# Performance work log

Hardware: AMD Instinct MI355X
Metric: run time of the kernel (lower is better)

Reference implementation:

```python
import jax, jax.numpy as jnp
import numpy as np

LABEL_SMOOTHING = 0.1
K_SLOPE = 5.0
N, D = 8192, 256


def setup_inputs() -> dict:
    key = jax.random.key(0)
    k1, k2, k3 = jax.random.split(key, 3)
    return {
        "image_features1": jax.random.normal(k1, (N, D), dtype=jnp.float32),
        "image_features2": jax.random.normal(k2, (N, D), dtype=jnp.float32),
        "logit_scale": jnp.asarray(14.2857, dtype=jnp.float32),  # ~ 1/0.07 CLIP temp
        "positive_weights": jax.random.normal(k3, (N,), dtype=jnp.float32),
    }


def _l2_normalize(x, axis=-1, eps=1e-12):
    # matches F.normalize(dim=-1)
    norm = jnp.linalg.norm(x, axis=axis, keepdims=True)
    return x / jnp.maximum(norm, eps)


def _weighted_infonce(sim, eps):
    # per row i: (1-eps_i)*(-sim[i,i] + lse_i) + eps_i*(-mean(sim[i,:]) + lse_i)
    #          = lse_i - (1-eps_i)*sim[i,i] - eps_i*mean_i
    n = sim.shape[0]
    lse = jax.nn.logsumexp(sim, axis=1)            # [n]
    diag = jnp.diagonal(sim)                       # [n]
    row_mean = jnp.mean(sim, axis=1)               # [n]
    per_row = lse - (1.0 - eps) * diag - eps * row_mean
    return jnp.sum(per_row) / n


def reference(image_features1, image_features2, logit_scale, positive_weights):
    f1 = _l2_normalize(image_features1)
    f2 = _l2_normalize(image_features2)
    logits12 = logit_scale * (f1 @ f2.T)           # [N, N]
    # eps = 1 - (1 - label_smoothing) * sigmoid(k * w)
    eps = 1.0 - (1.0 - LABEL_SMOOTHING) * jax.nn.sigmoid(K_SLOPE * positive_weights)
    loss1 = _weighted_infonce(logits12, eps)
    loss2 = _weighted_infonce(logits12.T, eps)
    return (loss1 + loss2) / 2.0
```

## Files before the change

kernel.cpp:

```cpp
#include <hip/hip_runtime.h>
#include <hip/hip_bf16.h>

#define NN 8192
#define DD 256
#define LOG2E 1.4426950408889634f
#define LN2f 0.6931471805599453f

typedef __attribute__((ext_vector_type(8))) short short8;
typedef __attribute__((ext_vector_type(4))) float f32x4;

__device__ __forceinline__ unsigned short f2bf(float x) {
    unsigned int u = __float_as_uint(x);
    u += 0x7fff + ((u >> 16) & 1);
    return (unsigned short)(u >> 16);
}
__device__ __forceinline__ float epsf(float w) {
    return 1.f - 0.9f / (1.f + __expf(-5.f * w));
}

__global__ __launch_bounds__(512) void nrm_kernel(
    const float* __restrict__ f1, const float* __restrict__ f2,
    const float* __restrict__ scale_p, const float* __restrict__ wts,
    unsigned short* __restrict__ f1n, unsigned short* __restrict__ f2n,
    float* __restrict__ diag, float* __restrict__ rse, float* __restrict__ cse,
    float4* __restrict__ STp, float* __restrict__ totalp)
{
    __shared__ float4 red[8][256];
    const int w = threadIdx.x >> 6, lane = threadIdx.x & 63;
    const float s = scale_p[0];
    const int row0 = blockIdx.x * 16 + w * 2;
    float s1a[4] = {0,0,0,0}, t1a[4] = {0,0,0,0};
    float s2a[4] = {0,0,0,0}, t2a[4] = {0,0,0,0};
#pragma unroll
    for (int r = 0; r < 2; ++r) {
        const int row = row0 + r;
        const float4 a = reinterpret_cast<const float4*>(f1 + (size_t)row * DD)[lane];
        const float4 b = reinterpret_cast<const float4*>(f2 + (size_t)row * DD)[lane];
        float sa = a.x * a.x + a.y * a.y + a.z * a.z + a.w * a.w;
        float sb = b.x * b.x + b.y * b.y + b.z * b.z + b.w * b.w;
        float sab = a.x * b.x + a.y * b.y + a.z * b.z + a.w * b.w;
#pragma unroll
        for (int off = 1; off < 64; off <<= 1) {
            sa += __shfl_xor(sa, off);
            sb += __shfl_xor(sb, off);
            sab += __shfl_xor(sab, off);
        }
        const float n1 = fmaxf(sqrtf(sa), 1e-12f);
        const float n2 = fmaxf(sqrtf(sb), 1e-12f);
        const float e = epsf(wts[row]);
        if (lane == 0) { diag[row] = s * sab / (n1 * n2); rse[row] = 0.f; cse[row] = 0.f; }
        const float r1 = s * LOG2E / n1, r2 = 1.0f / n2;
        const float v0 = a.x * r1, v1 = a.y * r1, v2 = a.z * r1, v3 = a.w * r1;
        const float u0 = b.x * r2, u1 = b.y * r2, u2 = b.z * r2, u3 = b.w * r2;
        ushort4 o1, o2;
        o1.x = f2bf(v0); o1.y = f2bf(v1); o1.z = f2bf(v2); o1.w = f2bf(v3);
        o2.x = f2bf(u0); o2.y = f2bf(u1); o2.z = f2bf(u2); o2.w = f2bf(u3);
        reinterpret_cast<ushort4*>(f1n + (size_t)row * DD)[lane] = o1;
        reinterpret_cast<ushort4*>(f2n + (size_t)row * DD)[lane] = o2;
        s1a[0] += v0; s1a[1] += v1; s1a[2] += v2; s1a[3] += v3;
        t1a[0] += e * v0; t1a[1] += e * v1; t1a[2] += e * v2; t1a[3] += e * v3;
        s2a[0] += u0; s2a[1] += u1; s2a[2] += u2; s2a[3] += u3;
        t2a[0] += e * u0; t2a[1] += e * u1; t2a[2] += e * u2; t2a[3] += e * u3;
    }
#pragma unroll
    for (int k = 0; k < 4; ++k)
        red[w][lane * 4 + k] = make_float4(s1a[k], t1a[k], s2a[k], t2a[k]);
    __syncthreads();
    if (threadIdx.x < 256) {
        const int c = threadIdx.x;
        float4 acc = red[0][c];
#pragma unroll
        for (int q = 1; q < 8; ++q) {
            const float4 v = red[q][c];
            acc.x += v.x; acc.y += v.y; acc.z += v.z; acc.w += v.w;
        }
        STp[blockIdx.x * 256 + c] = acc;
    }
    if (blockIdx.x == 0 && threadIdx.x == 0) totalp[0] = 0.f;
}

__global__ __launch_bounds__(256, 2) void gemm_kernel(
    const unsigned short* __restrict__ f1n, const unsigned short* __restrict__ f2n,
    float* __restrict__ rowsumexp, float* __restrict__ colsumexp)
{
    __shared__ char Bs[2][64 * 512];
    __shared__ float colbuf[2][1024];
    const int bid = blockIdx.x;
    const int bm = bid >> 3, bc = bid & 7;
    const int w = threadIdx.x >> 6, lane = threadIdx.x & 63;
    const int wr = (w >> 1) * 64, wc = (w & 1) * 32;
    const int lhi = lane >> 4, llo = lane & 15;

    const char* aBase = (const char*)f1n + ((size_t)(bm * 128 + wr + llo) * 512) + lhi * 16;
    short8 av[4][8];
#pragma unroll
    for (int m = 0; m < 4; ++m)
#pragma unroll
        for (int ks = 0; ks < 8; ++ks)
            av[m][ks] = *(const short8*)(aBase + (size_t)(m * 16) * 512 + ks * 64);
#pragma unroll
    for (int m = 0; m < 4; ++m)
#pragma unroll
        for (int ks = 0; ks < 8; ++ks)
            asm volatile("" : "+v"(av[m][ks]));

    const char* bBase = (const char*)f2n + (size_t)bc * 1024 * 512;

    auto stage = [&](int buf, int tile) {
#pragma unroll
        for (int i = 0; i < 8; ++i) {
            const int r = w * 16 + i * 2 + (lane >> 5);
            const int cs = (lane & 31) ^ (r & 15);
            __builtin_amdgcn_global_load_lds(
                (const __attribute__((address_space(1))) unsigned int*)
                    (bBase + (size_t)(tile * 64 + r) * 512 + cs * 16),
                (__attribute__((address_space(3))) unsigned int*)
                    (&Bs[buf][(w * 16 + i * 2) * 512]), 16, 0, 0);
        }
    };

    float rowpart[16];
#pragma unroll
    for (int i = 0; i < 16; ++i) rowpart[i] = 0.f;

    stage(0, 0);

    const int rb0 = wc + llo, rb1 = wc + 16 + llo;
    const int sw = llo << 4;

    for (int t = 0; t < 16; ++t) {
        const int cur = t & 1;
        if (t < 15) {
            stage(cur ^ 1, t + 1);
            asm volatile("s_waitcnt vmcnt(8)" ::: "memory");
        } else {
            asm volatile("s_waitcnt vmcnt(0)" ::: "memory");
        }
        __builtin_amdgcn_s_barrier();
        __builtin_amdgcn_sched_barrier(0);

        f32x4 acc[4][2];
#pragma unroll
        for (int m = 0; m < 4; ++m) {
            acc[m][0] = (f32x4){0.f, 0.f, 0.f, 0.f};
            acc[m][1] = (f32x4){0.f, 0.f, 0.f, 0.f};
        }
        const char* bs = Bs[cur];
#pragma unroll
        for (int ks = 0; ks < 8; ++ks) {
            const int kb = ks * 64 + lhi * 16;
            const short8 bv0 = *(const short8*)(bs + rb0 * 512 + (kb ^ sw));
            const short8 bv1 = *(const short8*)(bs + rb1 * 512 + (kb ^ sw));
#pragma unroll
            for (int m = 0; m < 4; ++m) {
                acc[m][0] = __builtin_amdgcn_mfma_f32_16x16x32_bf16(av[m][ks], bv0, acc[m][0], 0, 0, 0);
                acc[m][1] = __builtin_amdgcn_mfma_f32_16x16x32_bf16(av[m][ks], bv1, acc[m][1], 0, 0, 0);
            }
        }

        float cee0 = 0.f, cee1 = 0.f;
#pragma unroll
        for (int m = 0; m < 4; ++m)
#pragma unroll
            for (int j = 0; j < 4; ++j) {
                const float e0 = __builtin_exp2f(acc[m][0][j]);
                const float e1 = __builtin_exp2f(acc[m][1][j]);
                rowpart[m * 4 + j] += e0 + e1;
                cee0 += e0; cee1 += e1;
            }
        cee0 += __shfl_xor(cee0, 16); cee0 += __shfl_xor(cee0, 32);
        cee1 += __shfl_xor(cee1, 16); cee1 += __shfl_xor(cee1, 32);
        if (lhi == 0) {
            colbuf[w >> 1][t * 64 + wc + llo] = cee0;
            colbuf[w >> 1][t * 64 + wc + 16 + llo] = cee1;
        }
        __builtin_amdgcn_s_barrier();
    }

    __syncthreads();

#pragma unroll
    for (int m = 0; m < 4; ++m)
#pragma unroll
        for (int j = 0; j < 4; ++j) {
            float v = rowpart[m * 4 + j];
            v += __shfl_xor(v, 1); v += __shfl_xor(v, 2);
            v += __shfl_xor(v, 4); v += __shfl_xor(v, 8);
            if (llo == 0)
                atomicAdd(&rowsumexp[bm * 128 + wr + m * 16 + lhi * 4 + j], v);
        }
    for (int c = threadIdx.x; c < 1024; c += 256)
        atomicAdd(&colsumexp[bc * 1024 + c], colbuf[0][c] + colbuf[1][c]);
}

__global__ __launch_bounds__(256) void finA_kernel(
    const float* __restrict__ rse, const float* __restrict__ cse,
    const float* __restrict__ diag, const float* __restrict__ wts,
    const float4* __restrict__ STp, float4* __restrict__ P2,
    float* __restrict__ totalp)
{
    const int g = blockIdx.x, t = threadIdx.x;
    const int i = g * 256 + t;
    const float eps = epsf(wts[i]);
    float a = __logf(rse[i]) + __logf(cse[i]) - 2.f * (1.f - eps) * diag[i];
#pragma unroll
    for (int off = 1; off < 64; off <<= 1) a += __shfl_xor(a, off);
    __shared__ float red[4];
    if ((t & 63) == 0) red[t >> 6] = a;

    float4 s = make_float4(0.f, 0.f, 0.f, 0.f);
#pragma unroll 4
    for (int j = 0; j < 16; ++j) {
        const float4 v = STp[(g * 16 + j) * 256 + t];
        s.x += v.x; s.y += v.y; s.z += v.z; s.w += v.w;
    }
    P2[g * 256 + t] = s;

    __syncthreads();
    if (t == 0) atomicAdd(totalp, red[0] + red[1] + red[2] + red[3]);
}

__global__ __launch_bounds__(256) void fin_kernel(
    const float4* __restrict__ P2, const float* __restrict__ totalp,
    float* __restrict__ out)
{
    const int t = threadIdx.x;
    float4 s = make_float4(0.f, 0.f, 0.f, 0.f);
#pragma unroll 4
    for (int g = 0; g < 32; ++g) {
        const float4 v = P2[g * 256 + t];
        s.x += v.x; s.y += v.y; s.z += v.z; s.w += v.w;
    }
    float d = (s.y * s.z + s.x * s.w) * (LN2f / (float)NN);
#pragma unroll
    for (int off = 1; off < 64; off <<= 1) d += __shfl_xor(d, off);
    __shared__ float red[4];
    if ((t & 63) == 0) red[t >> 6] = d;
    __syncthreads();
    if (t == 0) {
        const float dot = red[0] + red[1] + red[2] + red[3];
        out[0] = (totalp[0] - dot) * (1.f / (2.f * (float)NN));
    }
}

extern "C" void kernel_launch(void* const* d_in, const int* in_sizes, int n_in,
                              void* d_out, int out_size, void* d_ws, size_t ws_size,
                              hipStream_t stream) {
    (void)in_sizes; (void)n_in; (void)out_size; (void)ws_size;
    const float* f1 = (const float*)d_in[0];
    const float* f2 = (const float*)d_in[1];
    const float* scale = (const float*)d_in[2];
    const float* wts = (const float*)d_in[3];
    float* out = (float*)d_out;

    char* ws = (char*)d_ws;
    unsigned short* f1n = (unsigned short*)ws;
    unsigned short* f2n = (unsigned short*)(ws + (size_t)4 * 1024 * 1024);
    float* fb = (float*)(ws + (size_t)8 * 1024 * 1024);
    float* rse    = fb;
    float* cse    = fb + 8192;
    float* diag   = fb + 16384;
    float* totalp = fb + 24576;
    float4* STp   = (float4*)(fb + 32768);
    float4* P2    = (float4*)(fb + 32768 + 524288);

    nrm_kernel<<<512, 512, 0, stream>>>(f1, f2, scale, wts, f1n, f2n,
                                        diag, rse, cse, STp, totalp);
    gemm_kernel<<<512, 256, 0, stream>>>(f1n, f2n, rse, cse);
    finA_kernel<<<32, 256, 0, stream>>>(rse, cse, diag, wts, STp, P2, totalp);
    fin_kernel<<<1, 256, 0, stream>>>(P2, totalp, out);
}
```

Baseline: 69.30 us.

## Give each wave a private B-tile pipeline to drop block-wide barriers

Each of the four waves now stages its own 16-row B sub-tile into a private double-buffered LDS slot and walks its own half of the block's 1024 columns across 32 steps. This removes the two per-iteration s_barrier calls and lets waves run independently, with loads issued two tiles ahead. In exchange the two waves sharing a column half each load B separately, and only one B fragment feeds the MFMA chain per step, so the MFMA-to-LDS-read ratio drops and global/LDS traffic for B doubles.

```diff
diff --git a/kernel.cpp b/kernel.cpp
--- a/kernel.cpp
+++ b/kernel.cpp
@@ -83,15 +83,16 @@
     const unsigned short* __restrict__ f1n, const unsigned short* __restrict__ f2n,
     float* __restrict__ rowsumexp, float* __restrict__ colsumexp)
 {
-    __shared__ char Bs[2][64 * 512];
+    __shared__ char Bs[4][2][16 * 512];
     __shared__ float colbuf[2][1024];
     const int bid = blockIdx.x;
     const int bm = bid >> 3, bc = bid & 7;
     const int w = threadIdx.x >> 6, lane = threadIdx.x & 63;
-    const int wr = (w >> 1) * 64, wc = (w & 1) * 32;
+    const int h = w >> 1;
+    const int cst = w & 1;
     const int lhi = lane >> 4, llo = lane & 15;
 
-    const char* aBase = (const char*)f1n + ((size_t)(bm * 128 + wr + llo) * 512) + lhi * 16;
+    const char* aBase = (const char*)f1n + ((size_t)(bm * 128 + h * 64 + llo) * 512) + lhi * 16;
     short8 av[4][8];
 #pragma unroll
     for (int m = 0; m < 4; ++m)
@@ -104,18 +105,20 @@
         for (int ks = 0; ks < 8; ++ks)
             asm volatile("" : "+v"(av[m][ks]));
 
-    const char* bBase = (const char*)f2n + (size_t)bc * 1024 * 512;
+    const char* bBase = (const char*)f2n + (size_t)(bc * 1024 + cst * 512) * 512;
 
     auto stage = [&](int buf, int tile) {
+        char* dst = &Bs[w][buf][0];
+        const char* src = bBase + (size_t)(tile * 16) * 512;
 #pragma unroll
         for (int i = 0; i < 8; ++i) {
-            const int r = w * 16 + i * 2 + (lane >> 5);
-            const int cs = (lane & 31) ^ (r & 15);
+            const int r = i * 2 + (lane >> 5);
+            const int cs = (lane & 31) ^ r;
             __builtin_amdgcn_global_load_lds(
                 (const __attribute__((address_space(1))) unsigned int*)
-                    (bBase + (size_t)(tile * 64 + r) * 512 + cs * 16),
+                    (src + (size_t)r * 512 + cs * 16),
                 (__attribute__((address_space(3))) unsigned int*)
-                    (&Bs[buf][(w * 16 + i * 2) * 512]), 16, 0, 0);
+                    (dst + i * 2 * 512), 16, 0, 0);
         }
     };
 
@@ -124,57 +127,43 @@
     for (int i = 0; i < 16; ++i) rowpart[i] = 0.f;
 
     stage(0, 0);
-
-    const int rb0 = wc + llo, rb1 = wc + 16 + llo;
+    stage(1, 1);
+
     const int sw = llo << 4;
 
-    for (int t = 0; t < 16; ++t) {
-        const int cur = t & 1;
-        if (t < 15) {
-            stage(cur ^ 1, t + 1);
+    for (int t = 0; t < 32; ++t) {
+        if (t < 31) {
             asm volatile("s_waitcnt vmcnt(8)" ::: "memory");
         } else {
             asm volatile("s_waitcnt vmcnt(0)" ::: "memory");
         }
-        __builtin_amdgcn_s_barrier();
-        __builtin_amdgcn_sched_barrier(0);
-
-        f32x4 acc[4][2];
-#pragma unroll
-        for (int m = 0; m < 4; ++m) {
-            acc[m][0] = (f32x4){0.f, 0.f, 0.f, 0.f};
-            acc[m][1] = (f32x4){0.f, 0.f, 0.f, 0.f};
-        }
-        const char* bs = Bs[cur];
+        const char* bs = &Bs[w][t & 1][0];
+
+        f32x4 acc[4];
+#pragma unroll
+        for (int m = 0; m < 4; ++m) acc[m] = (f32x4){0.f, 0.f, 0.f, 0.f};
 #pragma unroll
         for (int ks = 0; ks < 8; ++ks) {
             const int kb = ks * 64 + lhi * 16;
-            const short8 bv0 = *(const short8*)(bs + rb0 * 512 + (kb ^ sw));
-            const short8 bv1 = *(const short8*)(bs + rb1 * 512 + (kb ^ sw));
-#pragma unroll
-            for (int m = 0; m < 4; ++m) {
-                acc[m][0] = __builtin_amdgcn_mfma_f32_16x16x32_bf16(av[m][ks], bv0, acc[m][0], 0, 0, 0);
-                acc[m][1] = __builtin_amdgcn_mfma_f32_16x16x32_bf16(av[m][ks], bv1, acc[m][1], 0, 0, 0);
+            const short8 bv = *(const short8*)(bs + llo * 512 + (kb ^ sw));
+#pragma unroll
+            for (int m = 0; m < 4; ++m)
+                acc[m] = __builtin_amdgcn_mfma_f32_16x16x32_bf16(av[m][ks], bv, acc[m], 0, 0, 0);
+        }
+        asm volatile("s_waitcnt lgkmcnt(0)" ::: "memory");
+        if (t < 30) stage(t & 1, t + 2);
+
+        float cee = 0.f;
+#pragma unroll
+        for (int m = 0; m < 4; ++m)
+#pragma unroll
+            for (int j = 0; j < 4; ++j) {
+                const float e = __builtin_exp2f(acc[m][j]);
+                rowpart[m * 4 + j] += e;
+                cee += e;
             }
-        }
-
-        float cee0 = 0.f, cee1 = 0.f;
-#pragma unroll
-        for (int m = 0; m < 4; ++m)
-#pragma unroll
-            for (int j = 0; j < 4; ++j) {
-                const float e0 = __builtin_exp2f(acc[m][0][j]);
-                const float e1 = __builtin_exp2f(acc[m][1][j]);
-                rowpart[m * 4 + j] += e0 + e1;
-                cee0 += e0; cee1 += e1;
-            }
-        cee0 += __shfl_xor(cee0, 16); cee0 += __shfl_xor(cee0, 32);
-        cee1 += __shfl_xor(cee1, 16); cee1 += __shfl_xor(cee1, 32);
-        if (lhi == 0) {
-            colbuf[w >> 1][t * 64 + wc + llo] = cee0;
-            colbuf[w >> 1][t * 64 + wc + 16 + llo] = cee1;
-        }
-        __builtin_amdgcn_s_barrier();
+        cee += __shfl_xor(cee, 16); cee += __shfl_xor(cee, 32);
+        if (lhi == 0) colbuf[h][cst * 512 + t * 16 + llo] = cee;
     }
 
     __syncthreads();
@@ -187,7 +176,7 @@
             v += __shfl_xor(v, 1); v += __shfl_xor(v, 2);
             v += __shfl_xor(v, 4); v += __shfl_xor(v, 8);
             if (llo == 0)
-                atomicAdd(&rowsumexp[bm * 128 + wr + m * 16 + lhi * 4 + j], v);
+                atomicAdd(&rowsumexp[bm * 128 + h * 64 + m * 16 + lhi * 4 + j], v);
         }
     for (int c = threadIdx.x; c < 1024; c += 256)
         atomicAdd(&colsumexp[bc * 1024 + c], colbuf[0][c] + colbuf[1][c]);
```

After: 72.14 us. +4.1%, slower.
